# Kernel tuning notes

Hardware: AMD Instinct MI355X
Metric: run time of the kernel (lower is better)

Reference implementation:

```python
import jax, jax.numpy as jnp
import numpy as np

NUM_HEADS = 8
NUM_LANDMARKS = 64
TOPK_LANDMARKS = 4


def setup_inputs() -> dict:
    key = jax.random.key(0)
    k1, k2, k3, k4 = jax.random.split(key, 4)
    B, N, C = 1, 2048, 512
    return {
        "x": jax.random.normal(k1, (B, N, C), jnp.float32),
        "w_qkv": jax.random.normal(k2, (3 * C, C), jnp.float32) * 0.02,
        "w_proj": jax.random.normal(k3, (C, C), jnp.float32) * 0.02,
        "b_proj": jax.random.normal(k4, (C,), jnp.float32) * 0.02,
    }


def reference(x, w_qkv, w_proj, b_proj):
    B, N, C = x.shape
    H = NUM_HEADS
    Dh = C // H
    m = min(NUM_LANDMARKS, N)          # number of segments (torch views (B,H,m,seg,D))
    kl = min(TOPK_LANDMARKS, m)
    scale = Dh ** -0.5

    qkv = (x @ w_qkv.T).reshape(B, N, 3, H, Dh).transpose(2, 0, 3, 1, 4)
    q, k, v = qkv[0], qkv[1], qkv[2]   # each (B,H,N,Dh)

    seg = -(-N // m)                   # segment length = ceil(N/m)
    pad = seg * m - N

    def segmentize(t):
        if pad > 0:
            t = jnp.pad(t, ((0, 0), (0, 0), (0, pad), (0, 0)))
        return t.reshape(B, H, m, seg, Dh)

    k_seg = segmentize(k)              # (B,H,m,seg,Dh)
    v_seg = segmentize(v)

    centroids = k_seg.mean(axis=3)     # (B,H,m,Dh) -- includes pad zeros, as in torch
    route = jnp.einsum('bhnd,bhmd->bhnm', q, centroids) * scale
    _, topk_idx = jax.lax.top_k(route, kl)  # (B,H,N,kl)

    # gather routed segments per query: (B,H,N,kl,seg,Dh)
    gather = jax.vmap(jax.vmap(lambda segs, ix: segs[ix]))
    sel_k = gather(k_seg, topk_idx).reshape(B, H, N, kl * seg, Dh)
    sel_v = gather(v_seg, topk_idx).reshape(B, H, N, kl * seg, Dh)

    attn = jnp.einsum('bhnd,bhnkd->bhnk', q, sel_k) * scale
    attn = jax.nn.softmax(attn, axis=-1)
    out = jnp.einsum('bhnk,bhnkd->bhnd', attn, sel_v)  # (B,H,N,Dh)
    out = out.transpose(0, 2, 1, 3).reshape(B, N, C)
    return out @ w_proj.T + b_proj
```

## Files before the change

### kernel.cpp

```cpp
#include <hip/hip_runtime.h>
#include <hip/hip_bf16.h>
#include <math.h>

#define N_TOK 2048
#define C_DIM 512
#define H_NUM 8
#define DH 64
#define M_LM 64
#define SEG 32
#define KL 4
#define SCALE 0.125f

typedef __attribute__((ext_vector_type(8))) short short8;
typedef __attribute__((ext_vector_type(4))) short short4v;
typedef __attribute__((ext_vector_type(4))) float f32x4;

__device__ inline unsigned short f2bf(float f) {
  unsigned u = __float_as_uint(f);
  u += 0x7FFF + ((u >> 16) & 1);
  return (unsigned short)(u >> 16);
}
__device__ inline float bf2f(unsigned short h) {
  return __uint_as_float(((unsigned)h) << 16);
}

__global__ __launch_bounds__(256) void gemm_qk(
    const float* __restrict__ A, const float* __restrict__ B,
    float* __restrict__ out_q, float* __restrict__ out_k)
{
  __shared__ float As[32][68];
  __shared__ float Bs[32][68];
  int tid = threadIdx.x;
  int tx = tid & 15, ty = tid >> 4;
  int row0 = blockIdx.y << 6;
  int col0 = blockIdx.x << 6;
  float acc[4][4] = {};
  int kk = tid & 31, rr = tid >> 5;

  float pa[8], pb[8];
#pragma unroll
  for (int i = 0; i < 8; i++) {
    pa[i] = A[(size_t)(row0 + rr + i * 8) * 512 + kk];
    pb[i] = B[(size_t)(col0 + rr + i * 8) * 512 + kk];
  }

  for (int k0 = 0; k0 < 512; k0 += 32) {
    __syncthreads();
#pragma unroll
    for (int i = 0; i < 8; i++) {
      As[kk][rr + i * 8] = pa[i];
      Bs[kk][rr + i * 8] = pb[i];
    }
    __syncthreads();
    if (k0 + 32 < 512) {
#pragma unroll
      for (int i = 0; i < 8; i++) {
        pa[i] = A[(size_t)(row0 + rr + i * 8) * 512 + k0 + 32 + kk];
        pb[i] = B[(size_t)(col0 + rr + i * 8) * 512 + k0 + 32 + kk];
      }
    }
#pragma unroll
    for (int kk2 = 0; kk2 < 32; kk2++) {
      float a[4], b[4];
      *(float4*)a = *(const float4*)&As[kk2][ty << 2];
      *(float4*)b = *(const float4*)&Bs[kk2][tx << 2];
#pragma unroll
      for (int i = 0; i < 4; i++)
#pragma unroll
        for (int j = 0; j < 4; j++) acc[i][j] += a[i] * b[j];
    }
  }

  int t = col0 >> 9;
  int h = (col0 >> 6) & 7;
  float* dst = (t == 0) ? out_q : out_k;
#pragma unroll
  for (int i = 0; i < 4; i++) {
    int n = row0 + (ty << 2) + i;
#pragma unroll
    for (int j = 0; j < 4; j++) {
      int d = (tx << 2) + j;
      dst[(size_t)((h << 11) + n) * DH + d] = acc[i][j];
    }
  }
}

__global__ void split3_kernel(const float* __restrict__ x, const float* __restrict__ wv,
                              const float* __restrict__ wp,
                              unsigned short* __restrict__ X2,
                              unsigned short* __restrict__ W2v,
                              unsigned short* __restrict__ WP2)
{
  int idx = blockIdx.x * 256 + threadIdx.x;
  const float* src; unsigned short* dst; int li;
  if (idx < 1048576)      { src = x;  dst = X2;  li = idx; }
  else if (idx < 1310720) { src = wv; dst = W2v; li = idx - 1048576; }
  else                    { src = wp; dst = WP2; li = idx - 1310720; }
  int r = li >> 9, k = li & 511;
  float a = src[li];
  unsigned short h1 = f2bf(a);
  float r1 = a - bf2f(h1);
  dst[(size_t)(r << 10) + k] = h1;
  dst[(size_t)(r << 10) + 512 + k] = f2bf(r1);
}

__global__ __launch_bounds__(256) void gemm_mfma(
    const unsigned short* __restrict__ A2, const unsigned short* __restrict__ B2,
    float* __restrict__ ov, float* __restrict__ ofull,
    const float* __restrict__ bias, int ldout, int mode)
{
  __shared__ short Al[4096];
  __shared__ short Bl[4096];
  int tid = threadIdx.x;
  int lane = tid & 63, w = tid >> 6;
  int row0 = blockIdx.y << 6, col0 = blockIdx.x << 6;
  int wr = (w >> 1) * 32, wc = (w & 1) * 32;
  int m_lo = tid & 7, h8 = (tid >> 3) & 7, m_hi = tid >> 6;
  int ms = m_hi * 8 + m_lo;
  int q = lane >> 4, ln = lane & 15;

  f32x4 acc[2][2];
#pragma unroll
  for (int mi = 0; mi < 2; mi++)
#pragma unroll
    for (int ni = 0; ni < 2; ni++)
#pragma unroll
      for (int r = 0; r < 4; r++) acc[mi][ni][r] = 0.0f;

  for (int s = 0; s < 24; s++) {
    int ka = (s < 8) ? s * 64 : (s < 16) ? 512 + (s - 8) * 64 : (s - 16) * 64;
    int kb = (s < 8) ? s * 64 : (s < 16) ? (s - 8) * 64 : 512 + (s - 16) * 64;
    short8 a0 = *(const short8*)(A2 + (size_t)(row0 + ms) * 1024 + ka + h8 * 8);
    short8 a1 = *(const short8*)(A2 + (size_t)(row0 + ms + 32) * 1024 + ka + h8 * 8);
    short8 b0 = *(const short8*)(B2 + (size_t)(col0 + ms) * 1024 + kb + h8 * 8);
    short8 b1 = *(const short8*)(B2 + (size_t)(col0 + ms + 32) * 1024 + kb + h8 * 8);
    __syncthreads();
    *(short8*)&Al[(h8 * 64 + ms) * 8] = a0;
    *(short8*)&Al[(h8 * 64 + ms + 32) * 8] = a1;
    *(short8*)&Bl[(h8 * 64 + ms) * 8] = b0;
    *(short8*)&Bl[(h8 * 64 + ms + 32) * 8] = b1;
    __syncthreads();
    short8 af[2][2], bf[2][2];
#pragma unroll
    for (int sub = 0; sub < 2; sub++)
#pragma unroll
      for (int i = 0; i < 2; i++) {
        af[sub][i] = *(const short8*)&Al[((sub * 4 + q) * 64 + wr + i * 16 + ln) * 8];
        bf[sub][i] = *(const short8*)&Bl[((sub * 4 + q) * 64 + wc + i * 16 + ln) * 8];
      }
#pragma unroll
    for (int sub = 0; sub < 2; sub++)
#pragma unroll
      for (int mi = 0; mi < 2; mi++)
#pragma unroll
        for (int ni = 0; ni < 2; ni++)
          acc[mi][ni] = __builtin_amdgcn_mfma_f32_16x16x32_bf16(
              af[sub][mi], bf[sub][ni], acc[mi][ni], 0, 0, 0);
  }

  if (mode == 0) {
    int hh = (col0 >> 6) & 7;
#pragma unroll
    for (int mi = 0; mi < 2; mi++)
#pragma unroll
      for (int ni = 0; ni < 2; ni++)
#pragma unroll
        for (int r = 0; r < 4; r++) {
          int row = row0 + wr + mi * 16 + q * 4 + r;
          int d = wc + ni * 16 + ln;
          ov[(size_t)((hh << 11) + row) * DH + d] = acc[mi][ni][r];
        }
  } else {
#pragma unroll
    for (int mi = 0; mi < 2; mi++)
#pragma unroll
      for (int ni = 0; ni < 2; ni++)
#pragma unroll
        for (int r = 0; r < 4; r++) {
          int row = row0 + wr + mi * 16 + q * 4 + r;
          int col = col0 + wc + ni * 16 + ln;
          ofull[(size_t)row * ldout + col] = acc[mi][ni][r] + bias[col];
        }
  }
}

__global__ void centroid_kernel(const float* __restrict__ kb, float* __restrict__ cent)
{
  int idx = blockIdx.x * blockDim.x + threadIdx.x;
  int m = (idx >> 6) & 63;
  int h = idx >> 12;
  int d = idx & 63;
  const float* base = kb + ((size_t)(h << 11) + m * SEG) * DH + d;
  float s = 0.f;
#pragma unroll
  for (int ss = 0; ss < SEG; ss++) s += base[(size_t)ss * DH];
  cent[idx] = s * (1.0f / SEG);
}

__global__ __launch_bounds__(256) void route_topk_kernel(
    const float* __restrict__ qb, const float* __restrict__ cent, int* __restrict__ topk)
{
  __shared__ float centT[64][65];
  __shared__ float qs[4][64];
  int tid = threadIdx.x;
  int wave = tid >> 6, lane = tid & 63;
  int qi = (blockIdx.x << 2) + wave;
  int h = qi >> 11;
  qs[wave][lane] = qb[(size_t)qi * DH + lane];
  const float4* c4 = (const float4*)(cent + ((size_t)h << 12));
#pragma unroll
  for (int i = 0; i < 4; i++) {
    int f4 = tid + 256 * i;
    int m = f4 >> 4;
    int d0 = (f4 & 15) * 4;
    float4 v = c4[f4];
    centT[d0][m] = v.x; centT[d0 + 1][m] = v.y;
    centT[d0 + 2][m] = v.z; centT[d0 + 3][m] = v.w;
  }
  __syncthreads();
  float dot = 0.f;
#pragma unroll
  for (int d = 0; d < 64; d++) dot += qs[wave][d] * centT[d][lane];
  float val = dot * SCALE;
  for (int r = 0; r < KL; r++) {
    float v = val;
    int id = lane;
#pragma unroll
    for (int off = 32; off; off >>= 1) {
      float ov = __shfl_xor(v, off, 64);
      int oi = __shfl_xor(id, off, 64);
      if (ov > v || (ov == v && oi < id)) { v = ov; id = oi; }
    }
    if (lane == 0) topk[qi * KL + r] = id;
    if (lane == id) val = -INFINITY;
  }
}

__global__ void bin_kernel(const int* __restrict__ topk, int* __restrict__ cnt,
                           unsigned short* __restrict__ bucket)
{
  int qi = blockIdx.x * 256 + threadIdx.x;
  int4 tk = *(const int4*)(topk + qi * KL);
  int segs[4] = {tk.x, tk.y, tk.z, tk.w};
  int h = qi >> 11, n = qi & 2047;
#pragma unroll
  for (int r = 0; r < KL; r++) {
    int hs = (h << 6) | segs[r];
    int pos = atomicAdd(&cnt[hs], 1);
    bucket[hs * 2048 + pos] = (unsigned short)(n | (r << 11));
  }
}

__global__ void scan_kernel(const int* __restrict__ cnt, int* __restrict__ pref)
{
  __shared__ int s[512];
  int t = threadIdx.x;
  s[t] = (cnt[t] + 31) >> 5;
  __syncthreads();
  for (int off = 1; off < 512; off <<= 1) {
    int x = (t >= off) ? s[t - off] : 0;
    __syncthreads();
    s[t] += x;
    __syncthreads();
  }
  pref[t + 1] = s[t];
  if (t == 0) pref[0] = 0;
}

__global__ __launch_bounds__(256) void attend_mfma(
    const float* __restrict__ qb, const float* __restrict__ kb,
    const float* __restrict__ vb, const int* __restrict__ cnt,
    const unsigned short* __restrict__ bucket, const int* __restrict__ pref,
    float2* __restrict__ pml, float* __restrict__ po)
{
  __shared__ short Qs[16 * 32 * 8];
  __shared__ short Ks[16 * 32 * 8];
  __shared__ short Vt[8 * 64 * 8];
  __shared__ float Sl[32][36];
  __shared__ short P2[8 * 32 * 8];
  __shared__ int entL[32];
  int b = blockIdx.x;
  if (b >= pref[512]) return;
  int lo = 0, hi = 512;
  while (hi - lo > 1) { int mid = (lo + hi) >> 1; if (pref[mid] <= b) lo = mid; else hi = mid; }
  int hs = lo;
  int j = b - pref[hs];
  int h = hs >> 6, seg = hs & 63;
  int c = cnt[hs];
  int tid = threadIdx.x;

  if (tid < 32) {
    int i = j * 32 + tid;
    entL[tid] = (i < c) ? (int)bucket[hs * 2048 + i] : 0xFFFF;
  }
  {
    int row = tid & 31, part = tid >> 5;
    float x[8];
    const float* kr = kb + ((size_t)(h << 11) + seg * SEG + row) * DH + part * 8;
    *(float4*)&x[0] = *(const float4*)kr;
    *(float4*)&x[4] = *(const float4*)(kr + 4);
    short h8[8], l8[8];
#pragma unroll
    for (int q = 0; q < 8; q++) {
      unsigned short hb = f2bf(x[q]);
      h8[q] = hb; l8[q] = f2bf(x[q] - bf2f(hb));
    }
    *(short8*)&Ks[(part * 32 + row) * 8] = *(short8*)h8;
    *(short8*)&Ks[((8 + part) * 32 + row) * 8] = *(short8*)l8;
    const float* vr = vb + ((size_t)(h << 11) + seg * SEG + row) * DH + part * 8;
    *(float4*)&x[0] = *(const float4*)vr;
    *(float4*)&x[4] = *(const float4*)(vr + 4);
    int cdh = row >> 3, kj = row & 7;
#pragma unroll
    for (int q = 0; q < 8; q++) {
      int d = part * 8 + q;
      unsigned short hb = f2bf(x[q]);
      Vt[(cdh * 64 + d) * 8 + kj] = hb;
      Vt[((4 + cdh) * 64 + d) * 8 + kj] = f2bf(x[q] - bf2f(hb));
    }
  }
  __syncthreads();
  {
    int row = tid & 31, part = tid >> 5;
    int n = entL[row] & 2047;
    float x[8];
    const float* qr = qb + ((size_t)(h << 11) + n) * DH + part * 8;
    *(float4*)&x[0] = *(const float4*)qr;
    *(float4*)&x[4] = *(const float4*)(qr + 4);
    short h8[8], l8[8];
#pragma unroll
    for (int q = 0; q < 8; q++) {
      unsigned short hb = f2bf(x[q]);
      h8[q] = hb; l8[q] = f2bf(x[q] - bf2f(hb));
    }
    *(short8*)&Qs[(part * 32 + row) * 8] = *(short8*)h8;
    *(short8*)&Qs[((8 + part) * 32 + row) * 8] = *(short8*)l8;
  }
  __syncthreads();
  int w = tid >> 6, lane = tid & 63, ln = lane & 15, quad = lane >> 4;
  int m0 = (w & 1) * 16, n0 = (w >> 1) * 16;
  {
    f32x4 acc = {0.f, 0.f, 0.f, 0.f};
#pragma unroll
    for (int sidx = 0; sidx < 3; sidx++) {
      int qa = (sidx == 1) ? 8 : 0;
      int ka = (sidx == 2) ? 8 : 0;
#pragma unroll
      for (int kh = 0; kh < 2; kh++) {
        short8 a  = *(const short8*)&Qs[((qa + kh * 4 + quad) * 32 + m0 + ln) * 8];
        short8 bb = *(const short8*)&Ks[((ka + kh * 4 + quad) * 32 + n0 + ln) * 8];
        acc = __builtin_amdgcn_mfma_f32_16x16x32_bf16(a, bb, acc, 0, 0, 0);
      }
    }
#pragma unroll
    for (int r = 0; r < 4; r++)
      Sl[m0 + quad * 4 + r][n0 + ln] = acc[r] * SCALE;
  }
  __syncthreads();
  {
    int row = tid >> 3, c8 = tid & 7;
    float4 s4 = *(const float4*)&Sl[row][c8 * 4];
    float mx = fmaxf(fmaxf(s4.x, s4.y), fmaxf(s4.z, s4.w));
#pragma unroll
    for (int off = 1; off < 8; off <<= 1) mx = fmaxf(mx, __shfl_xor(mx, off, 64));
    float ev[4];
    ev[0] = expf(s4.x - mx); ev[1] = expf(s4.y - mx);
    ev[2] = expf(s4.z - mx); ev[3] = expf(s4.w - mx);
    float ls = ev[0] + ev[1] + ev[2] + ev[3];
#pragma unroll
    for (int off = 1; off < 8; off <<= 1) ls += __shfl_xor(ls, off, 64);
    short hh[4], llo[4];
#pragma unroll
    for (int q = 0; q < 4; q++) {
      unsigned short hb = f2bf(ev[q]);
      hh[q] = hb; llo[q] = f2bf(ev[q] - bf2f(hb));
    }
    int cd = c8 >> 1, koff = (c8 & 1) * 4;
    *(short4v*)&P2[(cd * 32 + row) * 8 + koff] = *(short4v*)hh;
    *(short4v*)&P2[((4 + cd) * 32 + row) * 8 + koff] = *(short4v*)llo;
    if (c8 == 0) {
      int e = entL[row];
      if (!(e & 0x8000)) {
        int qn = e & 2047, rr = (e >> 11) & 3;
        int p = (((h << 11) | qn) << 2) | rr;
        pml[p] = make_float2(mx, ls);
      }
    }
  }
  __syncthreads();
  {
    int n0c = (w >> 1) * 32;
    f32x4 accO[2];
#pragma unroll
    for (int t16 = 0; t16 < 2; t16++)
#pragma unroll
      for (int r = 0; r < 4; r++) accO[t16][r] = 0.f;
#pragma unroll
    for (int t16 = 0; t16 < 2; t16++) {
#pragma unroll
      for (int sidx = 0; sidx < 3; sidx++) {
        int pa = (sidx == 1) ? 4 : 0;
        int va = (sidx == 2) ? 4 : 0;
        short8 a  = *(const short8*)&P2[((pa + quad) * 32 + m0 + ln) * 8];
        short8 bb = *(const short8*)&Vt[((va + quad) * 64 + n0c + t16 * 16 + ln) * 8];
        accO[t16] = __builtin_amdgcn_mfma_f32_16x16x32_bf16(a, bb, accO[t16], 0, 0, 0);
      }
    }
#pragma unroll
    for (int t16 = 0; t16 < 2; t16++)
#pragma unroll
      for (int r = 0; r < 4; r++) {
        int row = m0 + quad * 4 + r;
        int e = entL[row];
        if (e & 0x8000) continue;
        int qn = e & 2047, rr = (e >> 11) & 3;
        int p = (((h << 11) | qn) << 2) | rr;
        po[(size_t)p * 64 + n0c + t16 * 16 + ln] = accO[t16][r];
      }
  }
}

__global__ void combine_kernel(const float2* __restrict__ pml,
                               const float* __restrict__ po,
                               unsigned short* __restrict__ ao2)
{
  int idx = blockIdx.x * 256 + threadIdx.x;
  int d = idx & 63;
  int qi = idx >> 6;
  int h = qi >> 11, n = qi & 2047;
  float2 ml0 = pml[qi * 4 + 0], ml1 = pml[qi * 4 + 1];
  float2 ml2 = pml[qi * 4 + 2], ml3 = pml[qi * 4 + 3];
  float M = fmaxf(fmaxf(ml0.x, ml1.x), fmaxf(ml2.x, ml3.x));
  float w0 = expf(ml0.x - M), w1 = expf(ml1.x - M);
  float w2 = expf(ml2.x - M), w3 = expf(ml3.x - M);
  float L = w0 * ml0.y + w1 * ml1.y + w2 * ml2.y + w3 * ml3.y;
  float o = w0 * po[(size_t)(qi * 4 + 0) * 64 + d]
          + w1 * po[(size_t)(qi * 4 + 1) * 64 + d]
          + w2 * po[(size_t)(qi * 4 + 2) * 64 + d]
          + w3 * po[(size_t)(qi * 4 + 3) * 64 + d];
  o /= L;
  unsigned short hb = f2bf(o);
  unsigned short lb = f2bf(o - bf2f(hb));
  size_t off0 = (size_t)n * 1024 + (h << 6) + d;
  ao2[off0] = hb;
  ao2[off0 + 512] = lb;
}

extern "C" void kernel_launch(void* const* d_in, const int* in_sizes, int n_in,
                              void* d_out, int out_size, void* d_ws, size_t ws_size,
                              hipStream_t stream)
{
  const float* x      = (const float*)d_in[0];
  const float* w_qkv  = (const float*)d_in[1];
  const float* w_proj = (const float*)d_in[2];
  const float* b_proj = (const float*)d_in[3];
  float* out = (float*)d_out;

  float* base = (float*)d_ws;
  float* qbuf = base;
  float* kbuf = base + 1048576;
  float* vbuf = base + 2097152;
  float* cent = base + 3145728;
  int*   topk = (int*)(base + 3178496);
  unsigned short* X2  = (unsigned short*)(base + 3244032);
  unsigned short* W2v = (unsigned short*)(base + 4292608);
  unsigned short* WP2 = (unsigned short*)(base + 4554752);
  unsigned short* AO2 = X2;
  int* cnt = (int*)(base + 4816896);
  unsigned short* bucket = (unsigned short*)(base + 4817408);
  float2* pml = (float2*)(base + 5341696);
  float* po   = base + 5472768;
  int* pref   = (int*)(base + 9667072);

  split3_kernel<<<6144, 256, 0, stream>>>(x, w_qkv + 1024 * 512, w_proj,
                                          X2, W2v, WP2);
  {
    dim3 grid(1024 / 64, N_TOK / 64);
    gemm_qk<<<grid, 256, 0, stream>>>(x, w_qkv, qbuf, kbuf);
  }
  {
    dim3 grid(512 / 64, N_TOK / 64);
    gemm_mfma<<<grid, 256, 0, stream>>>(X2, W2v, vbuf, nullptr, nullptr, 0, 0);
  }
  centroid_kernel<<<(H_NUM * M_LM * DH) / 256, 256, 0, stream>>>(kbuf, cent);
  route_topk_kernel<<<(H_NUM * N_TOK) / 4, 256, 0, stream>>>(qbuf, cent, topk);
  hipMemsetAsync(cnt, 0, 512 * sizeof(int), stream);
  bin_kernel<<<64, 256, 0, stream>>>(topk, cnt, bucket);
  scan_kernel<<<1, 512, 0, stream>>>(cnt, pref);
  attend_mfma<<<2560, 256, 0, stream>>>(qbuf, kbuf, vbuf, cnt, bucket, pref, pml, po);
  combine_kernel<<<4096, 256, 0, stream>>>(pml, po, AO2);
  {
    dim3 grid(C_DIM / 64, N_TOK / 64);
    gemm_mfma<<<grid, 256, 0, stream>>>(AO2, WP2, nullptr, out, b_proj, C_DIM, 1);
  }
}
```

Before: 210.8 us.

## Restructure fp32 QK GEMM to per-wave row tiles with swizzled B in LDS

Rewrites the fp32 Q/K projection GEMM so each wave owns 8 rows and each lane one output column. Only the weight tile is staged in shared memory, using an XOR swizzle to avoid bank conflicts, and A values are read as wave-uniform scalar loads straight from global memory. The grid doubles in the row dimension to 32-row blocks. The aim is to cut LDS traffic and register pressure, at the cost of loading the weight tile twice as often overall and relying on scalar/cache loads for A.

```diff
diff --git a/kernel.cpp b/kernel.cpp
--- a/kernel.cpp
+++ b/kernel.cpp
@@ -28,60 +28,48 @@
     const float* __restrict__ A, const float* __restrict__ B,
     float* __restrict__ out_q, float* __restrict__ out_k)
 {
-  __shared__ float As[32][68];
-  __shared__ float Bs[32][68];
+  __shared__ float Bs[64 * 64];
   int tid = threadIdx.x;
-  int tx = tid & 15, ty = tid >> 4;
-  int row0 = blockIdx.y << 6;
+  int lane = tid & 63;
+  int w = __builtin_amdgcn_readfirstlane(tid >> 6);
   int col0 = blockIdx.x << 6;
-  float acc[4][4] = {};
-  int kk = tid & 31, rr = tid >> 5;
-
-  float pa[8], pb[8];
-#pragma unroll
-  for (int i = 0; i < 8; i++) {
-    pa[i] = A[(size_t)(row0 + rr + i * 8) * 512 + kk];
-    pb[i] = B[(size_t)(col0 + rr + i * 8) * 512 + kk];
-  }
-
-  for (int k0 = 0; k0 < 512; k0 += 32) {
-    __syncthreads();
-#pragma unroll
-    for (int i = 0; i < 8; i++) {
-      As[kk][rr + i * 8] = pa[i];
-      Bs[kk][rr + i * 8] = pb[i];
-    }
-    __syncthreads();
-    if (k0 + 32 < 512) {
-#pragma unroll
-      for (int i = 0; i < 8; i++) {
-        pa[i] = A[(size_t)(row0 + rr + i * 8) * 512 + k0 + 32 + kk];
-        pb[i] = B[(size_t)(col0 + rr + i * 8) * 512 + k0 + 32 + kk];
-      }
-    }
-#pragma unroll
-    for (int kk2 = 0; kk2 < 32; kk2++) {
-      float a[4], b[4];
-      *(float4*)a = *(const float4*)&As[kk2][ty << 2];
-      *(float4*)b = *(const float4*)&Bs[kk2][tx << 2];
-#pragma unroll
-      for (int i = 0; i < 4; i++)
-#pragma unroll
-        for (int j = 0; j < 4; j++) acc[i][j] += a[i] * b[j];
-    }
-  }
-
+  int row0 = (blockIdx.y << 5) + (w << 3);
+  const float* Ab = A + (size_t)row0 * 512;
+  int scol = tid >> 2, spart = tid & 3;
+  const float* Bg = B + (size_t)(col0 + scol) * 512;
+
+  float acc[8] = {};
+  for (int k0 = 0; k0 < 512; k0 += 64) {
+    __syncthreads();
+#pragma unroll
+    for (int i = 0; i < 4; i++) {
+      int koff = spart * 4 + i * 16;
+      float4 v = *(const float4*)(Bg + k0 + koff);
+      int c4 = koff >> 2;
+      *(float4*)&Bs[scol * 64 + (((c4 ^ scol) & 15) << 2)] = v;
+    }
+    __syncthreads();
+#pragma unroll
+    for (int c4 = 0; c4 < 16; c4++) {
+      float4 bv = *(const float4*)&Bs[lane * 64 + (((c4 ^ lane) & 15) << 2)];
+      int kk = k0 + (c4 << 2);
+#pragma unroll
+      for (int r = 0; r < 8; r++) acc[r] += Ab[r * 512 + kk]     * bv.x;
+#pragma unroll
+      for (int r = 0; r < 8; r++) acc[r] += Ab[r * 512 + kk + 1] * bv.y;
+#pragma unroll
+      for (int r = 0; r < 8; r++) acc[r] += Ab[r * 512 + kk + 2] * bv.z;
+#pragma unroll
+      for (int r = 0; r < 8; r++) acc[r] += Ab[r * 512 + kk + 3] * bv.w;
+    }
+  }
   int t = col0 >> 9;
   int h = (col0 >> 6) & 7;
   float* dst = (t == 0) ? out_q : out_k;
 #pragma unroll
-  for (int i = 0; i < 4; i++) {
-    int n = row0 + (ty << 2) + i;
-#pragma unroll
-    for (int j = 0; j < 4; j++) {
-      int d = (tx << 2) + j;
-      dst[(size_t)((h << 11) + n) * DH + d] = acc[i][j];
-    }
+  for (int r = 0; r < 8; r++) {
+    int n = row0 + r;
+    dst[(size_t)((h << 11) + n) * DH + lane] = acc[r];
   }
 }
 
@@ -475,7 +463,7 @@
   split3_kernel<<<6144, 256, 0, stream>>>(x, w_qkv + 1024 * 512, w_proj,
                                           X2, W2v, WP2);
   {
-    dim3 grid(1024 / 64, N_TOK / 64);
+    dim3 grid(16, 64);
     gemm_qk<<<grid, 256, 0, stream>>>(x, w_qkv, qbuf, kbuf);
   }
   {
```

After: 246.0 us. 16.7% more time.

## Fold binning into top-k routing and drop scan via fixed per-segment grid

Applied to the files above, without the earlier changes.

Zeroing of the segment counters moves into the centroid kernel, and bucket insertion via atomics moves into the route/top-k kernel. This removes the memset, bin and scan launches and the topk buffer round trip. The attend kernel now uses a fixed grid of 8 blocks per head-segment that loop over 32-query chunks with stride 8, replacing the prefix-sum binary search. The trade-off is that many blocks exit immediately and heavily loaded segments are handled serially inside one block, which can cause load imbalance.

```diff
diff --git a/kernel.cpp b/kernel.cpp
--- a/kernel.cpp
+++ b/kernel.cpp
@@ -184,8 +184,13 @@
   }
 }
 
-__global__ void centroid_kernel(const float* __restrict__ kb, float* __restrict__ cent)
-{
+__global__ void centroid_kernel(const float* __restrict__ kb, float* __restrict__ cent,
+                                int* __restrict__ cnt)
+{
+  if (blockIdx.x == 0) {
+    cnt[threadIdx.x] = 0;
+    cnt[threadIdx.x + 256] = 0;
+  }
   int idx = blockIdx.x * blockDim.x + threadIdx.x;
   int m = (idx >> 6) & 63;
   int h = idx >> 12;
@@ -198,7 +203,8 @@
 }
 
 __global__ __launch_bounds__(256) void route_topk_kernel(
-    const float* __restrict__ qb, const float* __restrict__ cent, int* __restrict__ topk)
+    const float* __restrict__ qb, const float* __restrict__ cent,
+    int* __restrict__ cnt, unsigned short* __restrict__ bucket)
 {
   __shared__ float centT[64][65];
   __shared__ float qs[4][64];
@@ -222,6 +228,7 @@
 #pragma unroll
   for (int d = 0; d < 64; d++) dot += qs[wave][d] * centT[d][lane];
   float val = dot * SCALE;
+  int ids[KL];
   for (int r = 0; r < KL; r++) {
     float v = val;
     int id = lane;
@@ -231,46 +238,24 @@
       int oi = __shfl_xor(id, off, 64);
       if (ov > v || (ov == v && oi < id)) { v = ov; id = oi; }
     }
-    if (lane == 0) topk[qi * KL + r] = id;
+    ids[r] = id;
     if (lane == id) val = -INFINITY;
   }
-}
-
-__global__ void bin_kernel(const int* __restrict__ topk, int* __restrict__ cnt,
-                           unsigned short* __restrict__ bucket)
-{
-  int qi = blockIdx.x * 256 + threadIdx.x;
-  int4 tk = *(const int4*)(topk + qi * KL);
-  int segs[4] = {tk.x, tk.y, tk.z, tk.w};
-  int h = qi >> 11, n = qi & 2047;
-#pragma unroll
-  for (int r = 0; r < KL; r++) {
-    int hs = (h << 6) | segs[r];
-    int pos = atomicAdd(&cnt[hs], 1);
-    bucket[hs * 2048 + pos] = (unsigned short)(n | (r << 11));
-  }
-}
-
-__global__ void scan_kernel(const int* __restrict__ cnt, int* __restrict__ pref)
-{
-  __shared__ int s[512];
-  int t = threadIdx.x;
-  s[t] = (cnt[t] + 31) >> 5;
-  __syncthreads();
-  for (int off = 1; off < 512; off <<= 1) {
-    int x = (t >= off) ? s[t - off] : 0;
-    __syncthreads();
-    s[t] += x;
-    __syncthreads();
-  }
-  pref[t + 1] = s[t];
-  if (t == 0) pref[0] = 0;
+  if (lane == 0) {
+    int n = qi & 2047;
+#pragma unroll
+    for (int r = 0; r < KL; r++) {
+      int hs = (h << 6) | ids[r];
+      int pos = atomicAdd(&cnt[hs], 1);
+      bucket[hs * 2048 + pos] = (unsigned short)(n | (r << 11));
+    }
+  }
 }
 
 __global__ __launch_bounds__(256) void attend_mfma(
     const float* __restrict__ qb, const float* __restrict__ kb,
     const float* __restrict__ vb, const int* __restrict__ cnt,
-    const unsigned short* __restrict__ bucket, const int* __restrict__ pref,
+    const unsigned short* __restrict__ bucket,
     float2* __restrict__ pml, float* __restrict__ po)
 {
   __shared__ short Qs[16 * 32 * 8];
@@ -280,19 +265,12 @@
   __shared__ short P2[8 * 32 * 8];
   __shared__ int entL[32];
   int b = blockIdx.x;
-  if (b >= pref[512]) return;
-  int lo = 0, hi = 512;
-  while (hi - lo > 1) { int mid = (lo + hi) >> 1; if (pref[mid] <= b) lo = mid; else hi = mid; }
-  int hs = lo;
-  int j = b - pref[hs];
+  int hs = b >> 3, j0 = b & 7;
   int h = hs >> 6, seg = hs & 63;
   int c = cnt[hs];
+  if (j0 * 32 >= c) return;
   int tid = threadIdx.x;
 
-  if (tid < 32) {
-    int i = j * 32 + tid;
-    entL[tid] = (i < c) ? (int)bucket[hs * 2048 + i] : 0xFFFF;
-  }
   {
     int row = tid & 31, part = tid >> 5;
     float x[8];
@@ -320,103 +298,113 @@
     }
   }
   __syncthreads();
-  {
-    int row = tid & 31, part = tid >> 5;
-    int n = entL[row] & 2047;
-    float x[8];
-    const float* qr = qb + ((size_t)(h << 11) + n) * DH + part * 8;
-    *(float4*)&x[0] = *(const float4*)qr;
-    *(float4*)&x[4] = *(const float4*)(qr + 4);
-    short h8[8], l8[8];
-#pragma unroll
-    for (int q = 0; q < 8; q++) {
-      unsigned short hb = f2bf(x[q]);
-      h8[q] = hb; l8[q] = f2bf(x[q] - bf2f(hb));
-    }
-    *(short8*)&Qs[(part * 32 + row) * 8] = *(short8*)h8;
-    *(short8*)&Qs[((8 + part) * 32 + row) * 8] = *(short8*)l8;
-  }
-  __syncthreads();
+
   int w = tid >> 6, lane = tid & 63, ln = lane & 15, quad = lane >> 4;
   int m0 = (w & 1) * 16, n0 = (w >> 1) * 16;
-  {
-    f32x4 acc = {0.f, 0.f, 0.f, 0.f};
-#pragma unroll
-    for (int sidx = 0; sidx < 3; sidx++) {
-      int qa = (sidx == 1) ? 8 : 0;
-      int ka = (sidx == 2) ? 8 : 0;
-#pragma unroll
-      for (int kh = 0; kh < 2; kh++) {
-        short8 a  = *(const short8*)&Qs[((qa + kh * 4 + quad) * 32 + m0 + ln) * 8];
-        short8 bb = *(const short8*)&Ks[((ka + kh * 4 + quad) * 32 + n0 + ln) * 8];
-        acc = __builtin_amdgcn_mfma_f32_16x16x32_bf16(a, bb, acc, 0, 0, 0);
-      }
-    }
-#pragma unroll
-    for (int r = 0; r < 4; r++)
-      Sl[m0 + quad * 4 + r][n0 + ln] = acc[r] * SCALE;
-  }
-  __syncthreads();
-  {
-    int row = tid >> 3, c8 = tid & 7;
-    float4 s4 = *(const float4*)&Sl[row][c8 * 4];
-    float mx = fmaxf(fmaxf(s4.x, s4.y), fmaxf(s4.z, s4.w));
-#pragma unroll
-    for (int off = 1; off < 8; off <<= 1) mx = fmaxf(mx, __shfl_xor(mx, off, 64));
-    float ev[4];
-    ev[0] = expf(s4.x - mx); ev[1] = expf(s4.y - mx);
-    ev[2] = expf(s4.z - mx); ev[3] = expf(s4.w - mx);
-    float ls = ev[0] + ev[1] + ev[2] + ev[3];
-#pragma unroll
-    for (int off = 1; off < 8; off <<= 1) ls += __shfl_xor(ls, off, 64);
-    short hh[4], llo[4];
-#pragma unroll
-    for (int q = 0; q < 4; q++) {
-      unsigned short hb = f2bf(ev[q]);
-      hh[q] = hb; llo[q] = f2bf(ev[q] - bf2f(hb));
-    }
-    int cd = c8 >> 1, koff = (c8 & 1) * 4;
-    *(short4v*)&P2[(cd * 32 + row) * 8 + koff] = *(short4v*)hh;
-    *(short4v*)&P2[((4 + cd) * 32 + row) * 8 + koff] = *(short4v*)llo;
-    if (c8 == 0) {
-      int e = entL[row];
-      if (!(e & 0x8000)) {
-        int qn = e & 2047, rr = (e >> 11) & 3;
-        int p = (((h << 11) | qn) << 2) | rr;
-        pml[p] = make_float2(mx, ls);
-      }
-    }
-  }
-  __syncthreads();
-  {
-    int n0c = (w >> 1) * 32;
-    f32x4 accO[2];
-#pragma unroll
-    for (int t16 = 0; t16 < 2; t16++)
-#pragma unroll
-      for (int r = 0; r < 4; r++) accO[t16][r] = 0.f;
-#pragma unroll
-    for (int t16 = 0; t16 < 2; t16++) {
+
+  for (int j = j0; j * 32 < c; j += 8) {
+    if (tid < 32) {
+      int i = j * 32 + tid;
+      entL[tid] = (i < c) ? (int)bucket[hs * 2048 + i] : 0xFFFF;
+    }
+    __syncthreads();
+    {
+      int row = tid & 31, part = tid >> 5;
+      int n = entL[row] & 2047;
+      float x[8];
+      const float* qr = qb + ((size_t)(h << 11) + n) * DH + part * 8;
+      *(float4*)&x[0] = *(const float4*)qr;
+      *(float4*)&x[4] = *(const float4*)(qr + 4);
+      short h8[8], l8[8];
+#pragma unroll
+      for (int q = 0; q < 8; q++) {
+        unsigned short hb = f2bf(x[q]);
+        h8[q] = hb; l8[q] = f2bf(x[q] - bf2f(hb));
+      }
+      *(short8*)&Qs[(part * 32 + row) * 8] = *(short8*)h8;
+      *(short8*)&Qs[((8 + part) * 32 + row) * 8] = *(short8*)l8;
+    }
+    __syncthreads();
+    {
+      f32x4 acc = {0.f, 0.f, 0.f, 0.f};
 #pragma unroll
       for (int sidx = 0; sidx < 3; sidx++) {
-        int pa = (sidx == 1) ? 4 : 0;
-        int va = (sidx == 2) ? 4 : 0;
-        short8 a  = *(const short8*)&P2[((pa + quad) * 32 + m0 + ln) * 8];
-        short8 bb = *(const short8*)&Vt[((va + quad) * 64 + n0c + t16 * 16 + ln) * 8];
-        accO[t16] = __builtin_amdgcn_mfma_f32_16x16x32_bf16(a, bb, accO[t16], 0, 0, 0);
-      }
-    }
-#pragma unroll
-    for (int t16 = 0; t16 < 2; t16++)
-#pragma unroll
-      for (int r = 0; r < 4; r++) {
-        int row = m0 + quad * 4 + r;
+        int qa = (sidx == 1) ? 8 : 0;
+        int ka = (sidx == 2) ? 8 : 0;
+#pragma unroll
+        for (int kh = 0; kh < 2; kh++) {
+          short8 a  = *(const short8*)&Qs[((qa + kh * 4 + quad) * 32 + m0 + ln) * 8];
+          short8 bb = *(const short8*)&Ks[((ka + kh * 4 + quad) * 32 + n0 + ln) * 8];
+          acc = __builtin_amdgcn_mfma_f32_16x16x32_bf16(a, bb, acc, 0, 0, 0);
+        }
+      }
+#pragma unroll
+      for (int r = 0; r < 4; r++)
+        Sl[m0 + quad * 4 + r][n0 + ln] = acc[r] * SCALE;
+    }
+    __syncthreads();
+    {
+      int row = tid >> 3, c8 = tid & 7;
+      float4 s4 = *(const float4*)&Sl[row][c8 * 4];
+      float mx = fmaxf(fmaxf(s4.x, s4.y), fmaxf(s4.z, s4.w));
+#pragma unroll
+      for (int off = 1; off < 8; off <<= 1) mx = fmaxf(mx, __shfl_xor(mx, off, 64));
+      float ev[4];
+      ev[0] = expf(s4.x - mx); ev[1] = expf(s4.y - mx);
+      ev[2] = expf(s4.z - mx); ev[3] = expf(s4.w - mx);
+      float ls = ev[0] + ev[1] + ev[2] + ev[3];
+#pragma unroll
+      for (int off = 1; off < 8; off <<= 1) ls += __shfl_xor(ls, off, 64);
+      short hh[4], llo[4];
+#pragma unroll
+      for (int q = 0; q < 4; q++) {
+        unsigned short hb = f2bf(ev[q]);
+        hh[q] = hb; llo[q] = f2bf(ev[q] - bf2f(hb));
+      }
+      int cd = c8 >> 1, koff = (c8 & 1) * 4;
+      *(short4v*)&P2[(cd * 32 + row) * 8 + koff] = *(short4v*)hh;
+      *(short4v*)&P2[((4 + cd) * 32 + row) * 8 + koff] = *(short4v*)llo;
+      if (c8 == 0) {
         int e = entL[row];
-        if (e & 0x8000) continue;
-        int qn = e & 2047, rr = (e >> 11) & 3;
-        int p = (((h << 11) | qn) << 2) | rr;
-        po[(size_t)p * 64 + n0c + t16 * 16 + ln] = accO[t16][r];
-      }
+        if (!(e & 0x8000)) {
+          int qn = e & 2047, rr = (e >> 11) & 3;
+          int p = (((h << 11) | qn) << 2) | rr;
+          pml[p] = make_float2(mx, ls);
+        }
+      }
+    }
+    __syncthreads();
+    {
+      int n0c = (w >> 1) * 32;
+      f32x4 accO[2];
+#pragma unroll
+      for (int t16 = 0; t16 < 2; t16++)
+#pragma unroll
+        for (int r = 0; r < 4; r++) accO[t16][r] = 0.f;
+#pragma unroll
+      for (int t16 = 0; t16 < 2; t16++) {
+#pragma unroll
+        for (int sidx = 0; sidx < 3; sidx++) {
+          int pa = (sidx == 1) ? 4 : 0;
+          int va = (sidx == 2) ? 4 : 0;
+          short8 a  = *(const short8*)&P2[((pa + quad) * 32 + m0 + ln) * 8];
+          short8 bb = *(const short8*)&Vt[((va + quad) * 64 + n0c + t16 * 16 + ln) * 8];
+          accO[t16] = __builtin_amdgcn_mfma_f32_16x16x32_bf16(a, bb, accO[t16], 0, 0, 0);
+        }
+      }
+#pragma unroll
+      for (int t16 = 0; t16 < 2; t16++)
+#pragma unroll
+        for (int r = 0; r < 4; r++) {
+          int row = m0 + quad * 4 + r;
+          int e = entL[row];
+          if (e & 0x8000) continue;
+          int qn = e & 2047, rr = (e >> 11) & 3;
+          int p = (((h << 11) | qn) << 2) | rr;
+          po[(size_t)p * 64 + n0c + t16 * 16 + ln] = accO[t16][r];
+        }
+    }
+    __syncthreads();
   }
 }
 
@@ -461,7 +449,6 @@
   float* kbuf = base + 1048576;
   float* vbuf = base + 2097152;
   float* cent = base + 3145728;
-  int*   topk = (int*)(base + 3178496);
   unsigned short* X2  = (unsigned short*)(base + 3244032);
   unsigned short* W2v = (unsigned short*)(base + 4292608);
   unsigned short* WP2 = (unsigned short*)(base + 4554752);
@@ -470,7 +457,6 @@
   unsigned short* bucket = (unsigned short*)(base + 4817408);
   float2* pml = (float2*)(base + 5341696);
   float* po   = base + 5472768;
-  int* pref   = (int*)(base + 9667072);
 
   split3_kernel<<<6144, 256, 0, stream>>>(x, w_qkv + 1024 * 512, w_proj,
                                           X2, W2v, WP2);
@@ -482,12 +468,9 @@
     dim3 grid(512 / 64, N_TOK / 64);
     gemm_mfma<<<grid, 256, 0, stream>>>(X2, W2v, vbuf, nullptr, nullptr, 0, 0);
   }
-  centroid_kernel<<<(H_NUM * M_LM * DH) / 256, 256, 0, stream>>>(kbuf, cent);
-  route_topk_kernel<<<(H_NUM * N_TOK) / 4, 256, 0, stream>>>(qbuf, cent, topk);
-  hipMemsetAsync(cnt, 0, 512 * sizeof(int), stream);
-  bin_kernel<<<64, 256, 0, stream>>>(topk, cnt, bucket);
-  scan_kernel<<<1, 512, 0, stream>>>(cnt, pref);
-  attend_mfma<<<2560, 256, 0, stream>>>(qbuf, kbuf, vbuf, cnt, bucket, pref, pml, po);
+  centroid_kernel<<<(H_NUM * M_LM * DH) / 256, 256, 0, stream>>>(kbuf, cent, cnt);
+  route_topk_kernel<<<(H_NUM * N_TOK) / 4, 256, 0, stream>>>(qbuf, cent, cnt, bucket);
+  attend_mfma<<<4096, 256, 0, stream>>>(qbuf, kbuf, vbuf, cnt, bucket, pml, po);
   combine_kernel<<<4096, 256, 0, stream>>>(pml, po, AO2);
   {
     dim3 grid(C_DIM / 64, N_TOK / 64);
```

Result: slower. 261.9 us (+24.2%).
